# Optimization experiments

Hardware: AMD Instinct MI355X
Metric: run time of the kernel (lower is better)

Reference implementation:

```python
import jax, jax.numpy as jnp
import numpy as np

VN, BN, NSW, EC, MN = 64, 200, 10, 63, 73
FIN, HID = 32, 64
VLOW, VUPP = 0.9, 1.1


def _ln(z, eps=1e-5):
    m = jnp.mean(z, axis=-1, keepdims=True)
    v = jnp.var(z, axis=-1, keepdims=True)
    return (z - m) * jax.lax.rsqrt(v + eps)


def _layer(x, s, conn, deg_inv, Ws, Wi, Wj, U, Vw, first):
    # dense gated edge update over (B,V,V,H)
    e = jnp.einsum('bvwh,hk->bvwk', s, Ws) + (x @ Wi)[:, :, None, :] + (x @ Wj)[:, None, :, :]
    e = jax.nn.relu(_ln(e))
    s_out = e if first else s + e
    gate = jax.nn.sigmoid(s_out) * conn[None, :, :, None]
    msg = jnp.einsum('bvwh,bwh->bvh', gate, x @ Vw) * deg_inv[None, :, None]  # mean agg
    h = jax.nn.relu(_ln(x @ U + msg))
    return (h if first else x + h), s_out


def setup_inputs() -> dict:
    key = jax.random.key(0)
    ks = jax.random.split(key, 24)
    # radial feeder: path graph (line edges) + long-range tie switches, i<j (triu)
    ea = np.stack([np.arange(VN - 1), np.arange(1, VN)]).astype(np.int32)
    es = np.stack([np.arange(NSW), np.arange(NSW) + 32]).astype(np.int32)
    A = np.zeros((VN, VN), np.float32); A[ea[0], ea[1]] = 1; A[ea[1], ea[0]] = 1
    S = np.zeros((VN, VN), np.float32); S[es[0], es[1]] = 1; S[es[1], es[0]] = 1
    par = np.concatenate([ea[0], es[0]]); chi = np.concatenate([ea[1], es[1]])
    Incp = np.zeros((VN, MN), np.float32); Incp[par, np.arange(MN)] = 1
    Incc = np.zeros((VN, MN), np.float32); Incc[chi, np.arange(MN)] = 1
    deg = (A + S).sum(1)
    Dinv = np.diag((1.0 / np.maximum(deg, 1.0)).astype(np.float32))

    def w(k, shape):
        return jax.random.normal(k, shape, jnp.float32) / np.sqrt(shape[-2])

    return {
        'x': jax.random.normal(ks[0], (BN, VN, FIN), jnp.float32),
        'A': jnp.asarray(A), 'S': jnp.asarray(S),
        'embed_s': jax.random.normal(ks[1], (2, FIN), jnp.float32),
        'p0_Ws': w(ks[2], (FIN, HID)), 'p0_Wi': w(ks[3], (FIN, HID)),
        'p0_Wj': w(ks[4], (FIN, HID)), 'p0_U': w(ks[5], (FIN, HID)),
        'p0_V': w(ks[6], (FIN, HID)),
        'pl_Ws': w(ks[7], (2, HID, HID)), 'pl_Wi': w(ks[8], (2, HID, HID)),
        'pl_Wj': w(ks[9], (2, HID, HID)), 'pl_U': w(ks[10], (2, HID, HID)),
        'pl_V': w(ks[11], (2, HID, HID)),
        'smlp_W1': w(ks[12], (4 * HID, 4 * HID)), 'smlp_W2': w(ks[13], (4 * HID, 4)),
        'cmlp_W1': w(ks[14], (3 * HID, 3 * HID)), 'cmlp_W2': w(ks[15], (3 * HID, 3)),
        'Dinv': jnp.asarray(Dinv), 'Incp': jnp.asarray(Incp), 'Incc': jnp.asarray(Incc),
        'edge_A': jnp.asarray(ea), 'edge_S': jnp.asarray(es),
    }


def reference(x, A, S, embed_s, p0_Ws, p0_Wi, p0_Wj, p0_U, p0_V,
              pl_Ws, pl_Wi, pl_Wj, pl_U, pl_V,
              smlp_W1, smlp_W2, cmlp_W1, cmlp_W2,
              Dinv, Incp, Incc, edge_A, edge_S):
    B = x.shape[0]
    conn = jnp.clip(A + S, 0.0, 1.0)                       # (V,V) union adjacency
    deg_inv = 1.0 / jnp.maximum(conn.sum(1), 1.0)
    # init_embed_edges over dense S -> (B,V,V,FIN)
    s = jnp.broadcast_to(embed_s[S.astype(jnp.int32)][None], (B, VN, VN, FIN))
    xh, s = _layer(x, s, conn, deg_inv, p0_Ws, p0_Wi, p0_Wj, p0_U, p0_V, True)
    for l in range(pl_Ws.shape[0]):
        xh, s = _layer(xh, s, conn, deg_inv, pl_Ws[l], pl_Wi[l], pl_Wj[l], pl_U[l], pl_V[l], False)
    x_g = xh.sum(1)                                        # (B,H) graph feature

    # -- switch head (gather at triu switch edges, identical across batch) --
    si, sj = edge_S[0], edge_S[1]
    xg_s = jnp.broadcast_to(x_g[:, None, :], (B, si.shape[0], HID))
    smlp_in = jnp.concatenate([s[:, si, sj, :], xh[:, si], xh[:, sj], xg_s], axis=-1)
    smlp_out = jax.nn.sigmoid(jax.nn.relu(smlp_in @ smlp_W1) @ smlp_W2)  # (B,nsw,4)
    topology = smlp_out[..., 0]
    graph_topo = jnp.concatenate([jnp.ones((B, MN - NSW), x.dtype), topology], axis=1)
    ps = smlp_out[..., 1] - 0.5
    vs_p = VLOW * (1 - smlp_out[..., 2]) + VUPP * smlp_out[..., 2]
    vs_c = VLOW * (1 - smlp_out[..., 3]) + VUPP * smlp_out[..., 3]

    # -- connection head (gather at triu line edges) --
    ai, aj = edge_A[0], edge_A[1]
    xg_c = jnp.broadcast_to(x_g[:, None, :], (B, ai.shape[0], HID))
    cmlp_in = jnp.concatenate([xh[:, ai], xh[:, aj], xg_c], axis=-1)
    cmlp_out = jax.nn.sigmoid(jax.nn.relu(cmlp_in @ cmlp_W1) @ cmlp_W2)  # (B,Ec,3)
    pc = cmlp_out[..., 0] - 0.5
    vc_p = VLOW * (1 - cmlp_out[..., 1]) + VUPP * cmlp_out[..., 1]
    vc_c = VLOW * (1 - cmlp_out[..., 2]) + VUPP * cmlp_out[..., 2]

    # scatter into (B,M) physics tensors: first M-nsw cols from CMLP, last nsw from SMLP
    p_flow = jnp.concatenate([pc, ps], axis=1)
    v_par = jnp.concatenate([vc_p, vs_p], axis=1)
    v_chi = jnp.concatenate([vc_c, vs_c], axis=1)
    v = v_par @ (Dinv @ Incp).T + v_chi @ (Dinv @ Incc).T   # (B,V)
    v = v.at[:, 0].set(1.0)
    return jnp.concatenate([p_flow, v, graph_topo], axis=1)  # (B, M+V+M)
```

## Files before the change

kernel.cpp:

```cpp
#include <hip/hip_runtime.h>

#define BN 200
#define VN 64
#define HIDD 64
#define FINN 32
#define NSW 10
#define EC 63
#define MNE 73
#define NEDGE 146
#define NPACK 256

typedef unsigned short u16;
typedef unsigned int u32;
typedef _Float16 f16;
typedef __attribute__((ext_vector_type(8))) _Float16 f16x8;
typedef __attribute__((ext_vector_type(4))) float f32x4;

__device__ __forceinline__ float bfu(u16 u) { return __uint_as_float(((u32)u) << 16); }
__device__ __forceinline__ u16 f2bf(float f) {
    u32 x = __float_as_uint(f);
    u32 r = x + 0x7fffu + ((x >> 16) & 1u);
    return (u16)(r >> 16);
}
__device__ __forceinline__ float cvtv(const void* p, int i, int fl) {
    return fl ? bfu(((const u16*)p)[i]) : ((const float*)p)[i];
}

__device__ __forceinline__ int swzp(int row, int col) { return col ^ ((row & 7) << 2); }
__device__ __forceinline__ int swz16(int row, int col) { return col ^ ((row & 7) << 3); }

__device__ __forceinline__ float ldh(const u16* P, int i) {
    union { u16 u; f16 h; } c; c.u = P[i];
    return (float)c.h;
}
__device__ __forceinline__ void sth(u16* P, int i, float f) {
    union { u16 u; f16 h; } c; c.h = (f16)f;
    P[i] = c.u;
}
__device__ __forceinline__ u16 f2h(float f) {
    union { u16 u; f16 h; } c; c.h = (f16)f;
    return c.u;
}
__device__ __forceinline__ void unp2(u32 w, float& a, float& b) {
    union { u32 u; f16 h[2]; } c; c.u = w;
    a = (float)c.h[0]; b = (float)c.h[1];
}
__device__ __forceinline__ u32 pk2(float a, float b) {
    union { u32 u; f16 h[2]; } c; c.h[0] = (f16)a; c.h[1] = (f16)b;
    return c.u;
}
__device__ __forceinline__ f16x8 ldfragh(const u16* P, int i0) {
    return *(const f16x8*)&P[i0];
}

template <int CTRL>
__device__ __forceinline__ float dppadd(float x) {
    int v = __builtin_amdgcn_update_dpp(0, __float_as_int(x), CTRL, 0xf, 0xf, 1);
    return x + __int_as_float(v);
}
template <int N>
__device__ __forceinline__ float rlN(float x) {
    return __int_as_float(__builtin_amdgcn_readlane(__float_as_int(x), N));
}

__device__ __forceinline__ void lnpair(float p0, float p1, int isHi, float& o0, float& o1) {
    float s1 = p0 + p1;
    float s2 = fmaf(p0, p0, p1 * p1);
    s1 = dppadd<0x111>(s1); s1 = dppadd<0x112>(s1); s1 = dppadd<0x114>(s1); s1 = dppadd<0x118>(s1);
    s2 = dppadd<0x111>(s2); s2 = dppadd<0x112>(s2); s2 = dppadd<0x114>(s2); s2 = dppadd<0x118>(s2);
    float a1 = rlN<15>(s1) + rlN<31>(s1);
    float b1 = rlN<47>(s1) + rlN<63>(s1);
    float a2 = rlN<15>(s2) + rlN<31>(s2);
    float b2 = rlN<47>(s2) + rlN<63>(s2);
    float S1 = isHi ? b1 : a1;
    float S2 = isHi ? b2 : a2;
    float mean = S1 * 0.015625f;
    float var = fmaxf(S2 * 0.015625f - mean * mean, 0.f);
    float rn = rsqrtf(var + 1e-5f);
    o0 = fmaxf((p0 - mean) * rn, 0.f);
    o1 = fmaxf((p1 - mean) * rn, 0.f);
}

__device__ __forceinline__ float sigm(float x) {
    return __fdividef(1.f, 1.f + __expf(-x));
}

struct CvtArgs { const void* src[21]; };

__global__ __launch_bounds__(256) void k_prep(CvtArgs ca, const int* __restrict__ eA,
                                              const int* __restrict__ eS,
                                              u16* __restrict__ c1p, u16* __restrict__ c2p,
                                              u16* __restrict__ s1p, u16* __restrict__ s2p,
                                              u16* __restrict__ w0p, u16* __restrict__ wlp,
                                              float* __restrict__ ews, float* __restrict__ dinv,
                                              int* __restrict__ row_ptr, int* __restrict__ colp,
                                              int* __restrict__ sw_eidx,
                                              float* __restrict__ dinvD, int* __restrict__ incCnt,
                                              int* __restrict__ incM) {
    int t = threadIdx.x;
    int fl = (((const u16*)ca.src[1])[1] == 0x3F80) ? 1 : 0;
    if (blockIdx.x == 0) {
        __shared__ unsigned char flagL[64 * 65];
        __shared__ float wsL[FINN * 64];
        __shared__ float emL[64];
        __shared__ int degL[64], rpS[65], colS[NEDGE + 16];
        __shared__ int eAL[2 * EC], eSL[2 * NSW];

        if (t < 2 * EC) eAL[t] = eA[t];
        if (t >= 128 && t < 128 + 2 * NSW) eSL[t - 128] = eS[t - 128];
        if (t >= 160 && t < 224) emL[t - 160] = cvtv(ca.src[3], t - 160, fl);
        for (int i = t; i < FINN * 64; i += 256) wsL[i] = cvtv(ca.src[4], i, fl);
        for (int i = t; i < 4096; i += 256) {
            float a = cvtv(ca.src[1], i, fl);
            float s = cvtv(ca.src[2], i, fl);
            int r = i >> 6, c = i & 63;
            flagL[r * 65 + c] = (unsigned char)(((a != 0.f || s != 0.f) ? 1 : 0) |
                                                ((s != 0.f) ? 2 : 0));
        }
        __syncthreads();

        if (t < 128) {
            int j = t >> 6, k = t & 63;
            float a = 0.f;
#pragma unroll
            for (int h = 0; h < FINN; h++) a += emL[j * FINN + h] * wsL[h * 64 + k];
            ews[(j << 6) + k] = a;
        }
        if (t < 64) {
            int d = 0;
#pragma unroll
            for (int w = 0; w < 64; w++) d += flagL[t * 65 + w] & 1;
            degL[t] = d;
            dinv[t] = 1.f / fmaxf((float)d, 1.f);
        }
        __syncthreads();
        if (t == 0) {
            int c = 0;
            for (int v = 0; v < 64; v++) { rpS[v] = c; c += degL[v]; }
            rpS[64] = c;
        }
        __syncthreads();
        if (t < 65) row_ptr[t] = rpS[t];
        if (t < 64) {
            int pos = rpS[t];
#pragma unroll
            for (int w = 0; w < 64; w++) {
                int f = flagL[t * 65 + w];
                if (f & 1) colS[pos++] = w | ((f & 2) ? 256 : 0) | (t << 16);
            }
        }
        __syncthreads();
        int tot = rpS[64];
        if (t < tot) colp[t] = colS[t];
        if (t < NSW) {
            int si = eSL[t], sj = eSL[NSW + t];
            int idx = 0;
            for (int e = rpS[si]; e < rpS[si + 1]; e++)
                if ((colS[e] & 255) == sj) idx = e;
            sw_eidx[t] = idx;
        }
        if (t < 64) {
            dinvD[t] = cvtv(ca.src[18], t * 64 + t, fl);
            int cnt = 0;
            for (int m = 0; m < MNE; m++) {
                int par = (m < EC) ? eAL[m] : eSL[m - EC];
                int chi = (m < EC) ? eAL[EC + m] : eSL[NSW + (m - EC)];
                if (par == t && cnt < 8) incM[t * 8 + cnt++] = (m << 1);
                if (chi == t && cnt < 8) incM[t * 8 + cnt++] = (m << 1) | 1;
            }
            incCnt[t] = cnt;
        }
    } else {
        const int T1 = 36864, T2 = T1 + 3072, T3 = T2 + 65536, T4 = T3 + 4096;
        const int T5 = T4 + 8192, TOT = T5 + 40960;
        for (int i = (blockIdx.x - 1) * 256 + t; i < TOT; i += NPACK * 256) {
            int idx = i;
            const void* src;
            u16* dp;
            int K2, N2, nt, rem, loff = 0;
            if (idx < T1) {
                nt = idx / 3072; rem = idx - nt * 3072; src = ca.src[16];
                dp = c1p + idx; K2 = 192; N2 = 192;
            } else if (idx < T2) {
                idx -= T1; nt = 0; rem = idx; src = ca.src[17];
                dp = c2p + idx; K2 = 192; N2 = 3;
            } else if (idx < T3) {
                idx -= T2; nt = idx >> 12; rem = idx & 4095; src = ca.src[14];
                dp = s1p + idx; K2 = 256; N2 = 256;
            } else if (idx < T4) {
                idx -= T3; nt = 0; rem = idx; src = ca.src[15];
                dp = s2p + idx; K2 = 256; N2 = 4;
            } else if (idx < T5) {
                int j = idx - T4;
                int mt = j >> 11;
                int m2 = j & 2047;
                nt = m2 >> 9; rem = m2 & 511; src = ca.src[5 + mt];
                dp = w0p + j; K2 = 32; N2 = 64;
            } else {
                int j = idx - T5;
                int l = j / 20480;
                int jj = j - l * 20480;
                int mt = jj >> 12;
                int m2 = jj & 4095;
                nt = m2 >> 10; rem = m2 & 1023; src = ca.src[9 + mt];
                loff = l * 4096;
                dp = wlp + j; K2 = 64; N2 = 64;
            }
            int kb = rem >> 9, r8 = rem & 511, ln = r8 >> 3, jq = r8 & 7;
            int k = kb * 32 + ((ln >> 4) << 3) + jq;
            int n = nt * 16 + (ln & 15);
            float val = 0.f;
            if (n < N2 && k < K2) val = cvtv(src, loff + k * N2 + n, fl);
            *dp = f2h(val);
        }
    }
}

#define XI 0
#define XJ 1
#define XU 2
#define XV 3

__global__ __launch_bounds__(1024) void k_main(
    const void* __restrict__ xraw, const u16* __restrict__ A_u16,
    const int* __restrict__ eA, const int* __restrict__ eS,
    const float* __restrict__ ews, const float* __restrict__ dinv,
    const int* __restrict__ row_ptr, const int* __restrict__ colp,
    const int* __restrict__ sw_eidx,
    const float* __restrict__ dinvD, const int* __restrict__ incCnt, const int* __restrict__ incM,
    const u16* __restrict__ w0p, const u16* __restrict__ wlp,
    const u16* __restrict__ c1p, const u16* __restrict__ c2p,
    const u16* __restrict__ s1p, const u16* __restrict__ s2p,
    void* __restrict__ out_v)
{
    __shared__ __align__(16) u16 xPh[64 * 64];
    __shared__ __align__(16) u16 sPh[NEDGE * 64];
    __shared__ __align__(16) float preL[NEDGE * 64];
    __shared__ __align__(16) float tLs[4 * 64 * 64];
    __shared__ __align__(16) u16 xg16[64];
    __shared__ float ewsL[128];
    __shared__ float dinvL[64];
    __shared__ int rpL[65];
    __shared__ int colL[NEDGE + 6];
    __shared__ int swLx[NSW];
    __shared__ int eALs[2 * EC], eSLs[2 * NSW];
    __shared__ float cmoL[EC * 3], smoL[NSW * 4];

    int b = blockIdx.x, t = threadIdx.x;
    int lane = t & 63, wid = t >> 6;
    int m = lane & 15, quad = lane >> 4;
    int half = lane >> 5, hl = lane & 31, c2 = hl << 1;
    int fl = (A_u16[1] == 0x3F80) ? 1 : 0;

    {
        int i2 = t << 1;
        int r = i2 >> 5, c = i2 & 31;
        float va, vb;
        if (fl) {
            u32 wv = ((const u32*)xraw)[(size_t)b * 1024 + t];
            va = bfu((u16)(wv & 0xffffu));
            vb = bfu((u16)(wv >> 16));
        } else {
            float2 f = ((const float2*)xraw)[(size_t)b * 1024 + t];
            va = f.x; vb = f.y;
        }
        *(u32*)&xPh[(r << 6) + swz16(r, c)] = pk2(va, vb);
    }
    if (t < 128) ewsL[t] = ews[t];
    if (t < 64) dinvL[t] = dinv[t];
    if (t < 65) rpL[t] = row_ptr[t];
    if (t < NEDGE) colL[t] = colp[t];
    if (t < NSW) swLx[t] = sw_eidx[t];
    if (t >= 256 && t < 256 + 2 * EC) eALs[t - 256] = eA[t - 256];
    if (t >= 512 && t < 512 + 2 * NSW) eSLs[t - 512] = eS[t - 512];
    __syncthreads();

    {
        int mat = wid >> 2, Mt = wid & 3;
        const u16* bp = w0p + mat * 2048;
        int row = Mt * 16 + m;
        f16x8 a = ldfragh(xPh, (row << 6) + swz16(row, quad * 8));
        f32x4 acc[4];
#pragma unroll
        for (int nt = 0; nt < 4; nt++) {
            f16x8 bfr = ldfragh(bp, (nt << 9) + (lane << 3));
            acc[nt] = __builtin_amdgcn_mfma_f32_16x16x32_f16(a, bfr, (f32x4){0.f, 0.f, 0.f, 0.f}, 0, 0, 0);
        }
#pragma unroll
        for (int nt = 0; nt < 4; nt++)
#pragma unroll
            for (int r = 0; r < 4; r++) {
                int orow = Mt * 16 + quad * 4 + r;
                tLs[mat * 4096 + (orow << 6) + swzp(orow, nt * 16 + m)] = acc[nt][r];
            }
    }
    __syncthreads();

    for (int base = 0; base < NEDGE; base += 128) {
#pragma unroll
        for (int s = 0; s < 4; s++) {
            int q = (s << 1) + half;
            int e = base + wid + (q << 4);
            int ok = e < NEDGE;
            int ec = ok ? e : (NEDGE - 1);
            int cp = colL[ec];
            int w = cp & 255, v = (cp >> 16) & 255;
            float2 ew = *(const float2*)&ewsL[((((cp >> 8) & 1)) << 6) + c2];
            float2 xi = *(const float2*)&tLs[XI * 4096 + (v << 6) + swzp(v, c2)];
            float2 xj = *(const float2*)&tLs[XJ * 4096 + (w << 6) + swzp(w, c2)];
            float p0 = ew.x + xi.x + xj.x;
            float p1 = ew.y + xi.y + xj.y;
            float h0, h1;
            lnpair(p0, p1, half, h0, h1);
            float2 xv = *(const float2*)&tLs[XV * 4096 + (w << 6) + swzp(w, c2)];
            float2 g;
            g.x = xv.x * sigm(h0);
            g.y = xv.y * sigm(h1);
            if (ok) {
                *(u32*)&sPh[(ec << 6) + swz16(ec, c2)] = pk2(h0, h1);
                *(float2*)&preL[(ec << 6) + swzp(ec, c2)] = g;
            }
        }
    }
    __syncthreads();

    {
#pragma unroll
        for (int s = 0; s < 2; s++) {
            int v = (wid << 2) + (s << 1) + half;
            int r0 = rpL[v], r1 = rpL[v + 1];
            float m0 = 0.f, m1 = 0.f;
            for (int e = r0; e < r1; e++) {
                float2 p = *(const float2*)&preL[(e << 6) + swzp(e, c2)];
                m0 += p.x; m1 += p.y;
            }
            float2 xu = *(const float2*)&tLs[XU * 4096 + (v << 6) + swzp(v, c2)];
            float di = dinvL[v];
            float z0 = xu.x + m0 * di, z1 = xu.y + m1 * di;
            float h0, h1;
            lnpair(z0, z1, half, h0, h1);
            *(u32*)&xPh[(v << 6) + swz16(v, c2)] = pk2(h0, h1);
        }
    }
    __syncthreads();

    for (int l = 0; l < 2; l++) {
        {
            int mat = wid >> 2, Mt = wid & 3;
            const u16* bp = wlp + l * 20480 + (mat + 1) * 4096;
            int row = Mt * 16 + m;
            f32x4 acc[4];
#pragma unroll
            for (int nt = 0; nt < 4; nt++) acc[nt] = (f32x4){0.f, 0.f, 0.f, 0.f};
#pragma unroll
            for (int kb = 0; kb < 2; kb++) {
                f16x8 a = ldfragh(xPh, (row << 6) + swz16(row, kb * 32 + quad * 8));
#pragma unroll
                for (int nt = 0; nt < 4; nt++) {
                    f16x8 bfr = ldfragh(bp, (((nt << 1) + kb) << 9) + (lane << 3));
                    acc[nt] = __builtin_amdgcn_mfma_f32_16x16x32_f16(a, bfr, acc[nt], 0, 0, 0);
                }
            }
#pragma unroll
            for (int nt = 0; nt < 4; nt++)
#pragma unroll
                for (int r = 0; r < 4; r++) {
                    int orow = Mt * 16 + quad * 4 + r;
                    tLs[mat * 4096 + (orow << 6) + swzp(orow, nt * 16 + m)] = acc[nt][r];
                }

            const u16* sbp = wlp + l * 20480;
            for (int u = wid; u < 40; u += 16) {
                int rt = u >> 2, ntq = u & 3;
                int srow = rt * 16 + m;
                int ar = (srow > NEDGE - 1) ? (NEDGE - 1) : srow;
                f32x4 sacc = (f32x4){0.f, 0.f, 0.f, 0.f};
#pragma unroll
                for (int kb = 0; kb < 2; kb++) {
                    f16x8 a = ldfragh(sPh, (ar << 6) + swz16(ar, kb * 32 + quad * 8));
                    f16x8 bfr = ldfragh(sbp, (((ntq << 1) + kb) << 9) + (lane << 3));
                    sacc = __builtin_amdgcn_mfma_f32_16x16x32_f16(a, bfr, sacc, 0, 0, 0);
                }
#pragma unroll
                for (int r = 0; r < 4; r++) {
                    int orow = rt * 16 + quad * 4 + r;
                    if (orow < NEDGE)
                        preL[(orow << 6) + swzp(orow, ntq * 16 + m)] = sacc[r];
                }
            }
        }
        __syncthreads();

        for (int base = 0; base < NEDGE; base += 128) {
#pragma unroll
            for (int s = 0; s < 4; s++) {
                int q = (s << 1) + half;
                int e = base + wid + (q << 4);
                int ok = e < NEDGE;
                int ec = ok ? e : (NEDGE - 1);
                int cp = colL[ec];
                int w = cp & 255, v = (cp >> 16) & 255;
                int pidx = (ec << 6) + swzp(ec, c2);
                float2 pre = *(const float2*)&preL[pidx];
                float2 xi = *(const float2*)&tLs[XI * 4096 + (v << 6) + swzp(v, c2)];
                float2 xj = *(const float2*)&tLs[XJ * 4096 + (w << 6) + swzp(w, c2)];
                float p0 = pre.x + xi.x + xj.x;
                float p1 = pre.y + xi.y + xj.y;
                float h0, h1;
                lnpair(p0, p1, half, h0, h1);
                int hidx = (ec << 6) + swz16(ec, c2);
                float so0, so1;
                unp2(*(const u32*)&sPh[hidx], so0, so1);
                float n0 = so0 + h0, n1 = so1 + h1;
                float2 xv = *(const float2*)&tLs[XV * 4096 + (w << 6) + swzp(w, c2)];
                float2 g;
                g.x = xv.x * sigm(n0);
                g.y = xv.y * sigm(n1);
                if (ok) {
                    *(u32*)&sPh[hidx] = pk2(n0, n1);
                    *(float2*)&preL[pidx] = g;
                }
            }
        }
        __syncthreads();

        {
            float xa0 = 0.f, xa1 = 0.f;
#pragma unroll
            for (int s = 0; s < 2; s++) {
                int v = (wid << 2) + (s << 1) + half;
                int r0 = rpL[v], r1 = rpL[v + 1];
                float m0 = 0.f, m1 = 0.f;
                for (int e = r0; e < r1; e++) {
                    float2 p = *(const float2*)&preL[(e << 6) + swzp(e, c2)];
                    m0 += p.x; m1 += p.y;
                }
                float2 xu = *(const float2*)&tLs[XU * 4096 + (v << 6) + swzp(v, c2)];
                float di = dinvL[v];
                float z0 = xu.x + m0 * di, z1 = xu.y + m1 * di;
                float h0, h1;
                lnpair(z0, z1, half, h0, h1);
                int xi16 = (v << 6) + swz16(v, c2);
                float o0, o1;
                unp2(*(const u32*)&xPh[xi16], o0, o1);
                float x0 = o0 + h0, x1 = o1 + h1;
                *(u32*)&xPh[xi16] = pk2(x0, x1);
                xa0 += x0; xa1 += x1;
            }
            if (l == 1) {
                *(float2*)&tLs[(wid << 7) + (half << 6) + c2] = make_float2(xa0, xa1);
            }
        }
        __syncthreads();
    }

    if (t < 64) {
        float s = 0.f;
#pragma unroll
        for (int i = 0; i < 16; i++)
            s += tLs[(i << 7) + t] + tLs[(i << 7) + 64 + t];
        sth(xg16, t, s);
    }
    __syncthreads();

    u16* hcP = (u16*)tLs;
    u16* hsP = (u16*)tLs + 12288;

    if (wid < 12) {
        int Mt = wid & 3, ntg = wid >> 2;
        int e = Mt * 16 + m; if (e > 62) e = 62;
        int ai = eALs[e], aj = eALs[EC + e];
        f32x4 acc[4];
#pragma unroll
        for (int j = 0; j < 4; j++) acc[j] = (f32x4){0.f, 0.f, 0.f, 0.f};
#pragma unroll
        for (int kb = 0; kb < 6; kb++) {
            int k = kb * 32 + quad * 8;
            f16x8 a;
            if (k < 64) {
                a = ldfragh(xPh, (ai << 6) + swz16(ai, k));
            } else if (k < 128) {
                a = ldfragh(xPh, (aj << 6) + swz16(aj, k - 64));
            } else {
                a = ldfragh(xg16, k - 128);
            }
#pragma unroll
            for (int j = 0; j < 4; j++) {
                int nt = ntg * 4 + j;
                f16x8 bfr = ldfragh(c1p, ((nt * 6 + kb) << 9) + (lane << 3));
                acc[j] = __builtin_amdgcn_mfma_f32_16x16x32_f16(a, bfr, acc[j], 0, 0, 0);
            }
        }
#pragma unroll
        for (int j = 0; j < 4; j++) {
            int nt = ntg * 4 + j;
#pragma unroll
            for (int r = 0; r < 4; r++) {
                int row = Mt * 16 + quad * 4 + r;
                sth(hcP, row * 192 + swz16(row, nt * 16 + m), fmaxf(acc[j][r], 0.f));
            }
        }
    } else {
        int e2 = (m > 9) ? 9 : m;
        int si = eSLs[e2], sj = eSLs[NSW + e2];
        int sw = swLx[e2];
        f32x4 accS[4];
#pragma unroll
        for (int j = 0; j < 4; j++) accS[j] = (f32x4){0.f, 0.f, 0.f, 0.f};
#pragma unroll
        for (int kb = 0; kb < 8; kb++) {
            int k = kb * 32 + quad * 8;
            f16x8 a;
            if (k < 64) {
                a = ldfragh(sPh, (sw << 6) + swz16(sw, k));
            } else if (k < 128) {
                a = ldfragh(xPh, (si << 6) + swz16(si, k - 64));
            } else if (k < 192) {
                a = ldfragh(xPh, (sj << 6) + swz16(sj, k - 128));
            } else {
                a = ldfragh(xg16, k - 192);
            }
#pragma unroll
            for (int j = 0; j < 4; j++) {
                int nt = (wid - 12) * 4 + j;
                f16x8 bfr = ldfragh(s1p, ((nt * 8 + kb) << 9) + (lane << 3));
                accS[j] = __builtin_amdgcn_mfma_f32_16x16x32_f16(a, bfr, accS[j], 0, 0, 0);
            }
        }
#pragma unroll
        for (int j = 0; j < 4; j++) {
            int nt = (wid - 12) * 4 + j;
#pragma unroll
            for (int r = 0; r < 4; r++) {
                int row = quad * 4 + r;
                sth(hsP, (row << 8) + swz16(row, nt * 16 + m), fmaxf(accS[j][r], 0.f));
            }
        }
    }
    __syncthreads();

    if (wid < 4) {
        f32x4 accD = (f32x4){0.f, 0.f, 0.f, 0.f};
        int row = wid * 16 + m;
#pragma unroll
        for (int kb = 0; kb < 6; kb++) {
            f16x8 a = ldfragh(hcP, row * 192 + swz16(row, kb * 32 + quad * 8));
            f16x8 bfr = ldfragh(c2p, (kb << 9) + (lane << 3));
            accD = __builtin_amdgcn_mfma_f32_16x16x32_f16(a, bfr, accD, 0, 0, 0);
        }
#pragma unroll
        for (int r = 0; r < 4; r++) {
            int row2 = wid * 16 + quad * 4 + r;
            if (row2 < EC && m < 3)
                cmoL[row2 * 3 + m] = 1.f / (1.f + __expf(-accD[r]));
        }
    } else if (wid == 4) {
        f32x4 accT = (f32x4){0.f, 0.f, 0.f, 0.f};
#pragma unroll
        for (int kb = 0; kb < 8; kb++) {
            f16x8 a = ldfragh(hsP, (m << 8) + swz16(m, kb * 32 + quad * 8));
            f16x8 bfr = ldfragh(s2p, (kb << 9) + (lane << 3));
            accT = __builtin_amdgcn_mfma_f32_16x16x32_f16(a, bfr, accT, 0, 0, 0);
        }
#pragma unroll
        for (int r = 0; r < 4; r++) {
            int row = quad * 4 + r;
            if (row < NSW && m < 4)
                smoL[row * 4 + m] = 1.f / (1.f + __expf(-accT[r]));
        }
    }
    __syncthreads();

    if (t < 2 * MNE + VN) {
        float val;
        if (t < MNE) {
            val = (t < EC) ? cmoL[t * 3] - 0.5f : smoL[(t - EC) * 4 + 1] - 0.5f;
        } else if (t < MNE + VN) {
            int i = t - MNE;
            if (i == 0) {
                val = 1.0f;
            } else {
                float acc = 0.f;
                int c = incCnt[i];
                for (int q = 0; q < c; q++) {
                    int em = incM[i * 8 + q];
                    int mm = em >> 1, role = em & 1;
                    float vv = (mm < EC) ? 0.9f + 0.2f * cmoL[mm * 3 + 1 + role]
                                         : 0.9f + 0.2f * smoL[(mm - EC) * 4 + 2 + role];
                    acc += vv;
                }
                val = acc * dinvD[i];
            }
        } else {
            int mm = t - (MNE + VN);
            val = (mm < EC) ? 1.0f : smoL[(mm - EC) * 4];
        }
        size_t oidx = (size_t)b * (2 * MNE + VN) + t;
        if (fl) ((u16*)out_v)[oidx] = f2bf(val);
        else    ((float*)out_v)[oidx] = val;
    }
}

extern "C" void kernel_launch(void* const* d_in, const int* in_sizes, int n_in,
                              void* d_out, int out_size, void* d_ws, size_t ws_size,
                              hipStream_t stream) {
    const int* eA = (const int*)d_in[21];
    const int* eS = (const int*)d_in[22];

    float* pool = (float*)d_ws;
    float* ews     = pool;
    float* dinv    = ews + 128;
    float* dinvD   = dinv + 64;
    int*   row_ptr = (int*)(dinvD + 64);
    int*   colp    = row_ptr + 80;
    int*   sw_eidx = colp + 256;
    int*   incCnt  = sw_eidx + 16;
    int*   incM    = incCnt + 64;
    u16*   c1p = (u16*)(incM + 512);
    u16*   c2p = c1p + 36864;
    u16*   s1p = c2p + 3072;
    u16*   s2p = s1p + 65536;
    u16*   w0p = s2p + 4096;
    u16*   wlp = w0p + 8192;

    CvtArgs ca;
    for (int i = 0; i < 21; i++) ca.src[i] = d_in[i];

    k_prep<<<1 + NPACK, 256, 0, stream>>>(ca, eA, eS,
                                          c1p, c2p, s1p, s2p, w0p, wlp,
                                          ews, dinv, row_ptr, colp, sw_eidx,
                                          dinvD, incCnt, incM);

    k_main<<<BN, 1024, 0, stream>>>(d_in[0], (const u16*)d_in[1], eA, eS,
                                    ews, dinv, row_ptr, colp, sw_eidx,
                                    dinvD, incCnt, incM,
                                    w0p, wlp, c1p, c2p, s1p, s2p,
                                    d_out);
}
```

Baseline: 149.0 us.

## Fuse per-edge gated update into per-node aggregation loop, dropping a barrier

Moves edge-feature computation (layernorm, sigmoid gate, state write) into the per-node CSR aggregation loop, so each node computes its incident edges' messages directly. This removes a separate edge pass, an LDS round-trip through preL and a __syncthreads per layer. A separate scratch buffer holds the graph-sum partials because tLs is still being read. The edge work is now distributed per node, which may add load imbalance across threads.

```diff
diff --git a/kernel.cpp b/kernel.cpp
--- a/kernel.cpp
+++ b/kernel.cpp
@@ -29,10 +29,6 @@
 __device__ __forceinline__ int swzp(int row, int col) { return col ^ ((row & 7) << 2); }
 __device__ __forceinline__ int swz16(int row, int col) { return col ^ ((row & 7) << 3); }
 
-__device__ __forceinline__ float ldh(const u16* P, int i) {
-    union { u16 u; f16 h; } c; c.u = P[i];
-    return (float)c.h;
-}
 __device__ __forceinline__ void sth(u16* P, int i, float f) {
     union { u16 u; f16 h; } c; c.h = (f16)f;
     P[i] = c.u;
@@ -237,6 +233,7 @@
     __shared__ __align__(16) u16 sPh[NEDGE * 64];
     __shared__ __align__(16) float preL[NEDGE * 64];
     __shared__ __align__(16) float tLs[4 * 64 * 64];
+    __shared__ __align__(16) float xgScr[16 * 128];
     __shared__ __align__(16) u16 xg16[64];
     __shared__ float ewsL[128];
     __shared__ float dinvL[64];
@@ -296,47 +293,30 @@
     }
     __syncthreads();
 
-    for (int base = 0; base < NEDGE; base += 128) {
-#pragma unroll
-        for (int s = 0; s < 4; s++) {
-            int q = (s << 1) + half;
-            int e = base + wid + (q << 4);
-            int ok = e < NEDGE;
-            int ec = ok ? e : (NEDGE - 1);
-            int cp = colL[ec];
-            int w = cp & 255, v = (cp >> 16) & 255;
-            float2 ew = *(const float2*)&ewsL[((((cp >> 8) & 1)) << 6) + c2];
-            float2 xi = *(const float2*)&tLs[XI * 4096 + (v << 6) + swzp(v, c2)];
-            float2 xj = *(const float2*)&tLs[XJ * 4096 + (w << 6) + swzp(w, c2)];
-            float p0 = ew.x + xi.x + xj.x;
-            float p1 = ew.y + xi.y + xj.y;
-            float h0, h1;
-            lnpair(p0, p1, half, h0, h1);
-            float2 xv = *(const float2*)&tLs[XV * 4096 + (w << 6) + swzp(w, c2)];
-            float2 g;
-            g.x = xv.x * sigm(h0);
-            g.y = xv.y * sigm(h1);
-            if (ok) {
-                *(u32*)&sPh[(ec << 6) + swz16(ec, c2)] = pk2(h0, h1);
-                *(float2*)&preL[(ec << 6) + swzp(ec, c2)] = g;
-            }
-        }
-    }
-    __syncthreads();
-
     {
 #pragma unroll
         for (int s = 0; s < 2; s++) {
             int v = (wid << 2) + (s << 1) + half;
             int r0 = rpL[v], r1 = rpL[v + 1];
+            float2 xi2 = *(const float2*)&tLs[XI * 4096 + (v << 6) + swzp(v, c2)];
             float m0 = 0.f, m1 = 0.f;
             for (int e = r0; e < r1; e++) {
-                float2 p = *(const float2*)&preL[(e << 6) + swzp(e, c2)];
-                m0 += p.x; m1 += p.y;
-            }
-            float2 xu = *(const float2*)&tLs[XU * 4096 + (v << 6) + swzp(v, c2)];
+                int cp = colL[e];
+                int w = cp & 255;
+                float2 ew2 = *(const float2*)&ewsL[((((cp >> 8) & 1)) << 6) + c2];
+                float2 xj2 = *(const float2*)&tLs[XJ * 4096 + (w << 6) + swzp(w, c2)];
+                float p0 = ew2.x + xi2.x + xj2.x;
+                float p1 = ew2.y + xi2.y + xj2.y;
+                float h0, h1;
+                lnpair(p0, p1, half, h0, h1);
+                *(u32*)&sPh[(e << 6) + swz16(e, c2)] = pk2(h0, h1);
+                float2 xv2 = *(const float2*)&tLs[XV * 4096 + (w << 6) + swzp(w, c2)];
+                m0 += xv2.x * sigm(h0);
+                m1 += xv2.y * sigm(h1);
+            }
+            float2 xu2 = *(const float2*)&tLs[XU * 4096 + (v << 6) + swzp(v, c2)];
             float di = dinvL[v];
-            float z0 = xu.x + m0 * di, z1 = xu.y + m1 * di;
+            float z0 = xu2.x + m0 * di, z1 = xu2.y + m1 * di;
             float h0, h1;
             lnpair(z0, z1, half, h0, h1);
             *(u32*)&xPh[(v << 6) + swz16(v, c2)] = pk2(h0, h1);
@@ -391,53 +371,35 @@
         }
         __syncthreads();
 
-        for (int base = 0; base < NEDGE; base += 128) {
-#pragma unroll
-            for (int s = 0; s < 4; s++) {
-                int q = (s << 1) + half;
-                int e = base + wid + (q << 4);
-                int ok = e < NEDGE;
-                int ec = ok ? e : (NEDGE - 1);
-                int cp = colL[ec];
-                int w = cp & 255, v = (cp >> 16) & 255;
-                int pidx = (ec << 6) + swzp(ec, c2);
-                float2 pre = *(const float2*)&preL[pidx];
-                float2 xi = *(const float2*)&tLs[XI * 4096 + (v << 6) + swzp(v, c2)];
-                float2 xj = *(const float2*)&tLs[XJ * 4096 + (w << 6) + swzp(w, c2)];
-                float p0 = pre.x + xi.x + xj.x;
-                float p1 = pre.y + xi.y + xj.y;
-                float h0, h1;
-                lnpair(p0, p1, half, h0, h1);
-                int hidx = (ec << 6) + swz16(ec, c2);
-                float so0, so1;
-                unp2(*(const u32*)&sPh[hidx], so0, so1);
-                float n0 = so0 + h0, n1 = so1 + h1;
-                float2 xv = *(const float2*)&tLs[XV * 4096 + (w << 6) + swzp(w, c2)];
-                float2 g;
-                g.x = xv.x * sigm(n0);
-                g.y = xv.y * sigm(n1);
-                if (ok) {
-                    *(u32*)&sPh[hidx] = pk2(n0, n1);
-                    *(float2*)&preL[pidx] = g;
-                }
-            }
-        }
-        __syncthreads();
-
         {
             float xa0 = 0.f, xa1 = 0.f;
 #pragma unroll
             for (int s = 0; s < 2; s++) {
                 int v = (wid << 2) + (s << 1) + half;
                 int r0 = rpL[v], r1 = rpL[v + 1];
+                float2 xi2 = *(const float2*)&tLs[XI * 4096 + (v << 6) + swzp(v, c2)];
                 float m0 = 0.f, m1 = 0.f;
                 for (int e = r0; e < r1; e++) {
-                    float2 p = *(const float2*)&preL[(e << 6) + swzp(e, c2)];
-                    m0 += p.x; m1 += p.y;
+                    int cp = colL[e];
+                    int w = cp & 255;
+                    float2 pre = *(const float2*)&preL[(e << 6) + swzp(e, c2)];
+                    float2 xj2 = *(const float2*)&tLs[XJ * 4096 + (w << 6) + swzp(w, c2)];
+                    float p0 = pre.x + xi2.x + xj2.x;
+                    float p1 = pre.y + xi2.y + xj2.y;
+                    float h0, h1;
+                    lnpair(p0, p1, half, h0, h1);
+                    int hidx = (e << 6) + swz16(e, c2);
+                    float so0, so1;
+                    unp2(*(const u32*)&sPh[hidx], so0, so1);
+                    float n0 = so0 + h0, n1 = so1 + h1;
+                    *(u32*)&sPh[hidx] = pk2(n0, n1);
+                    float2 xv2 = *(const float2*)&tLs[XV * 4096 + (w << 6) + swzp(w, c2)];
+                    m0 += xv2.x * sigm(n0);
+                    m1 += xv2.y * sigm(n1);
                 }
-                float2 xu = *(const float2*)&tLs[XU * 4096 + (v << 6) + swzp(v, c2)];
+                float2 xu2 = *(const float2*)&tLs[XU * 4096 + (v << 6) + swzp(v, c2)];
                 float di = dinvL[v];
-                float z0 = xu.x + m0 * di, z1 = xu.y + m1 * di;
+                float z0 = xu2.x + m0 * di, z1 = xu2.y + m1 * di;
                 float h0, h1;
                 lnpair(z0, z1, half, h0, h1);
                 int xi16 = (v << 6) + swz16(v, c2);
@@ -447,9 +409,8 @@
                 *(u32*)&xPh[xi16] = pk2(x0, x1);
                 xa0 += x0; xa1 += x1;
             }
-            if (l == 1) {
-                *(float2*)&tLs[(wid << 7) + (half << 6) + c2] = make_float2(xa0, xa1);
-            }
+            if (l == 1)
+                *(float2*)&xgScr[(wid << 7) + (half << 6) + c2] = make_float2(xa0, xa1);
         }
         __syncthreads();
     }
@@ -458,7 +419,7 @@
         float s = 0.f;
 #pragma unroll
         for (int i = 0; i < 16; i++)
-            s += tLs[(i << 7) + t] + tLs[(i << 7) + 64 + t];
+            s += xgScr[(i << 7) + t] + xgScr[(i << 7) + 64 + t];
         sth(xg16, t, s);
     }
     __syncthreads();
```

Result: no change. 149.9 us (+0.6%).
